# Kernel optimization log

Measured on AMD Instinct MI355X. Metric: run time of the kernel, lower is better.

Reference implementation:

```python
import jax, jax.numpy as jnp
import numpy as np

NUM_USERS = 50000
NUM_ITEMS = 100000
TOTAL_NODES = NUM_USERS + NUM_ITEMS
EMBED_DIM = 128
NUM_LAYERS = 2
NUM_EDGES = 2000000
REL_WEIGHTS = (1.0, 0.5, 2.0)  # rel_weight dict values, fixed order


def setup_inputs() -> dict:
    key = jax.random.key(0)
    ks = jax.random.split(key, 7)
    # Xavier-uniform embedding table
    bound = np.sqrt(6.0 / (TOTAL_NODES + EMBED_DIM))
    emb = jax.random.uniform(ks[0], (TOTAL_NODES, EMBED_DIM), jnp.float32, -bound, bound)
    inp = {"emb": emb}
    for r in range(3):
        inp[f"src_r{r}"] = jax.random.randint(ks[1 + 2 * r], (NUM_EDGES,), 0, TOTAL_NODES, jnp.int32)
        inp[f"dst_r{r}"] = jax.random.randint(ks[2 + 2 * r], (NUM_EDGES,), 0, TOTAL_NODES, jnp.int32)
    return inp


def _propagate(x, srcs, dsts):
    # One layer: agg = mean over relations of w_r * SpMM_r(x), where
    # SparseTensor(row=src, col=dst).matmul(x) => out[src] += x[dst]
    agg = jnp.zeros_like(x)
    for w, src, dst in zip(REL_WEIGHTS, srcs, dsts):
        msg = jax.ops.segment_sum(x[dst], src, num_segments=TOTAL_NODES)
        agg = agg + w * msg
    return agg / len(REL_WEIGHTS)


def reference(emb, src_r0, dst_r0, src_r1, dst_r1, src_r2, dst_r2):
    srcs = (src_r0, src_r1, src_r2)
    dsts = (dst_r0, dst_r1, dst_r2)
    x = emb
    all_embs = [x]
    for _ in range(NUM_LAYERS):
        x = _propagate(x, srcs, dsts)
        all_embs.append(x)
    z = jnp.mean(jnp.stack(all_embs, axis=1), axis=1)  # [N, D]
    users_emb = z[:NUM_USERS]
    items_emb = z[NUM_USERS:NUM_USERS + NUM_ITEMS]
    return users_emb, items_emb
```

## Files before the change

### kernel.cpp

```cpp
#include <hip/hip_runtime.h>
#include <hip/hip_fp16.h>

#define TOTAL_NODES 150000
#define EMBED_DIM   128
#define NUM_EDGES   2000000
#define N_ELEM      (TOTAL_NODES * EMBED_DIM)

#define NGRP     37
#define GCAP     180224
#define EPB1     4096
#define NBKT     2344
#define NBKT_PAD 2368
#define SCAP2    2944
#define P2BLK    44
#define BS_NODES 64

typedef float vf2 __attribute__((ext_vector_type(2)));
typedef float vf4 __attribute__((ext_vector_type(4)));

__global__ void convert_kernel(const float* __restrict__ in, __half* __restrict__ outh,
                               int* __restrict__ gcur, int* __restrict__ bcur) {
    const int n4 = N_ELEM / 4;
    const int stride = gridDim.x * blockDim.x;
    const int gid = blockIdx.x * blockDim.x + threadIdx.x;
    if (gid < NGRP) gcur[gid] = 0;
    if (gid < NBKT_PAD) bcur[gid] = 0;
    for (int i = gid; i < n4; i += stride) {
        float4 v = reinterpret_cast<const float4*>(in)[i];
        union { __half2 h[2]; vf2 f; } u;
        u.h[0] = __float22half2_rn({v.x, v.y});
        u.h[1] = __float22half2_rn({v.z, v.w});
        __builtin_nontemporal_store(u.f, reinterpret_cast<vf2*>(outh) + i);
    }
}

__global__ __launch_bounds__(256) void split1(const int* __restrict__ s0, const int* __restrict__ d0,
                                              const int* __restrict__ s1, const int* __restrict__ d1,
                                              const int* __restrict__ s2, const int* __restrict__ d2,
                                              int* __restrict__ gcur, unsigned int* __restrict__ gbuf) {
    const int rel   = blockIdx.x >> 9;
    const int inner = blockIdx.x & 511;
    const int base  = inner * EPB1;
    const int ne    = min(EPB1, NUM_EDGES - base);
    if (ne <= 0) return;
    const int* sp = (rel == 0) ? s0 : ((rel == 1) ? s1 : s2);
    const int* dp = (rel == 0) ? d0 : ((rel == 1) ? d1 : d2);

    __shared__ int cnt[NGRP], excl[NGRP], bas[NGRP], rc[NGRP];
    __shared__ unsigned int stage[EPB1];
    __shared__ unsigned char grp[EPB1];
    const int t = threadIdx.x;
    for (int i = t; i < NGRP; i += 256) cnt[i] = 0;
    __syncthreads();

    unsigned int pay[16];
    int pg[16];
    #pragma unroll
    for (int q = 0; q < 4; ++q) {
        const int idx = (q * 256 + t) * 4;
        if (idx < ne) {
            const int4 s4 = *reinterpret_cast<const int4*>(sp + base + idx);
            const int4 d4 = *reinterpret_cast<const int4*>(dp + base + idx);
            const int ss[4] = {s4.x, s4.y, s4.z, s4.w};
            const int dd[4] = {d4.x, d4.y, d4.z, d4.w};
            #pragma unroll
            for (int k = 0; k < 4; ++k) {
                const int g = ss[k] >> 12;
                pay[q * 4 + k] = ((unsigned int)(ss[k] & 4095) << 20) |
                                 ((unsigned int)dd[k] << 2) | (unsigned int)rel;
                pg[q * 4 + k] = g;
                atomicAdd(&cnt[g], 1);
            }
        }
    }
    __syncthreads();
    if (t == 0) { int run = 0; for (int i = 0; i < NGRP; ++i) { excl[i] = run; run += cnt[i]; } }
    __syncthreads();
    if (t < NGRP) { if (cnt[t] > 0) bas[t] = atomicAdd(&gcur[t], cnt[t]); rc[t] = excl[t]; }
    __syncthreads();
    #pragma unroll
    for (int q = 0; q < 4; ++q) {
        const int idx = (q * 256 + t) * 4;
        if (idx < ne) {
            #pragma unroll
            for (int k = 0; k < 4; ++k) {
                const int g = pg[q * 4 + k];
                const int pos = atomicAdd(&rc[g], 1);
                stage[pos] = pay[q * 4 + k];
                grp[pos] = (unsigned char)g;
            }
        }
    }
    __syncthreads();
    for (int j = t; j < ne; j += 256) {
        const int g = grp[j];
        const int o = bas[g] + (j - excl[g]);
        if (o < GCAP) gbuf[(size_t)g * GCAP + o] = stage[j];
    }
}

__global__ __launch_bounds__(256) void split2(const int* __restrict__ gcur,
                                              const unsigned int* __restrict__ gbuf,
                                              int* __restrict__ bcur, unsigned int* __restrict__ buf2) {
    const int g     = blockIdx.x / P2BLK;
    const int inner = blockIdx.x % P2BLK;
    const int gsz   = min(gcur[g], GCAP);
    const int base  = inner * EPB1;
    if (base >= gsz) return;
    const int ne = min(EPB1, gsz - base);
    const unsigned int* src = gbuf + (size_t)g * GCAP + base;

    __shared__ int cnt[64], excl[64], bas2[64], rc[64];
    __shared__ unsigned int stage[EPB1];
    const int t = threadIdx.x;
    if (t < 64) cnt[t] = 0;
    __syncthreads();

    unsigned int pay[16];
    #pragma unroll
    for (int q = 0; q < 4; ++q) {
        const int idx = (q * 256 + t) * 4;
        if (idx + 4 <= ne) {
            const uint4 v = *reinterpret_cast<const uint4*>(src + idx);
            pay[q * 4 + 0] = v.x; pay[q * 4 + 1] = v.y;
            pay[q * 4 + 2] = v.z; pay[q * 4 + 3] = v.w;
            atomicAdd(&cnt[(v.x >> 26) & 63], 1);
            atomicAdd(&cnt[(v.y >> 26) & 63], 1);
            atomicAdd(&cnt[(v.z >> 26) & 63], 1);
            atomicAdd(&cnt[(v.w >> 26) & 63], 1);
        } else {
            #pragma unroll
            for (int k = 0; k < 4; ++k) {
                if (idx + k < ne) {
                    const unsigned int p = src[idx + k];
                    pay[q * 4 + k] = p;
                    atomicAdd(&cnt[(p >> 26) & 63], 1);
                }
            }
        }
    }
    __syncthreads();
    if (t == 0) { int run = 0; for (int i = 0; i < 64; ++i) { excl[i] = run; run += cnt[i]; } }
    __syncthreads();
    if (t < 64) { if (cnt[t] > 0) bas2[t] = atomicAdd(&bcur[g * 64 + t], cnt[t]); rc[t] = excl[t]; }
    __syncthreads();
    #pragma unroll
    for (int q = 0; q < 4; ++q) {
        const int idx = (q * 256 + t) * 4;
        #pragma unroll
        for (int k = 0; k < 4; ++k) {
            if (idx + k < ne) {
                const unsigned int p = pay[q * 4 + k];
                const int pos = atomicAdd(&rc[(p >> 26) & 63], 1);
                stage[pos] = p;
            }
        }
    }
    __syncthreads();
    for (int j = t; j < ne; j += 256) {
        const unsigned int p = stage[j];
        const int bb = (p >> 26) & 63;
        const int o = bas2[bb] + (j - excl[bb]);
        if (o < SCAP2) buf2[(size_t)(g * 64 + bb) * SCAP2 + o] = p;
    }
}

template <int MODE>
__global__ __launch_bounds__(256) void pull_kernel(const __half* __restrict__ xh,
                                                   const int* __restrict__ bcur,
                                                   const unsigned int* __restrict__ buf2,
                                                   const float* __restrict__ embf,
                                                   __half* __restrict__ aggh,
                                                   float* __restrict__ outf) {
    __shared__ unsigned int sorted[SCAP2];
    __shared__ int cnt[64], cur[64], noff[65];
    const int b = blockIdx.x, t = threadIdx.x;
    const int c = min(bcur[b], SCAP2);
    const unsigned int* rb = buf2 + (size_t)b * SCAP2;
    if (t < 64) cnt[t] = 0;
    __syncthreads();
    for (int i = t; i < c; i += 256) atomicAdd(&cnt[(rb[i] >> 20) & 63], 1);
    __syncthreads();
    if (t == 0) { int run = 0; for (int i = 0; i < 64; ++i) { noff[i] = run; run += cnt[i]; } noff[64] = run; }
    __syncthreads();
    if (t < 64) cur[t] = noff[t];
    __syncthreads();
    for (int i = t; i < c; i += 256) {
        const unsigned int p = rb[i];
        const int pos = atomicAdd(&cur[(p >> 20) & 63], 1);
        sorted[pos] = p & 0xFFFFFu;
    }
    __syncthreads();

    const int hw = t >> 5, lane = t & 31;
    const int sub = lane >> 4, ch = lane & 15;
    const char* xb = reinterpret_cast<const char*>(xh) + (ch << 4);
    union F4H { vf4 f; __half2 h[4]; };
    const float c1 = 1.f / 3.f, c2 = 1.f / 9.f, c3 = 1.f / 27.f;

#define EDGE_FMA(P, W, ACC0, ACC1) do {                                         \
        F4H _u; _u.f = *reinterpret_cast<const vf4*>(xb + ((size_t)((P) >> 2) << 8)); \
        float2 _x0 = __half22float2(_u.h[0]), _x1 = __half22float2(_u.h[1]);    \
        float2 _x2 = __half22float2(_u.h[2]), _x3 = __half22float2(_u.h[3]);    \
        ACC0.x = fmaf(W, _x0.x, ACC0.x); ACC0.y = fmaf(W, _x0.y, ACC0.y);       \
        ACC0.z = fmaf(W, _x1.x, ACC0.z); ACC0.w = fmaf(W, _x1.y, ACC0.w);       \
        ACC1.x = fmaf(W, _x2.x, ACC1.x); ACC1.y = fmaf(W, _x2.y, ACC1.y);       \
        ACC1.z = fmaf(W, _x3.x, ACC1.z); ACC1.w = fmaf(W, _x3.y, ACC1.w);       \
    } while (0)
#define REL_W(P) ((((P) & 3u) == 1u) ? 0.5f : ((((P) & 3u) == 2u) ? 2.0f : 1.0f))

    for (int ln = hw; ln < BS_NODES; ln += 8) {
        const int node = b * BS_NODES + ln;
        if (node >= TOTAL_NODES) break;
        vf4 a0 = {0.f, 0.f, 0.f, 0.f}, b0 = {0.f, 0.f, 0.f, 0.f};
        vf4 a1 = {0.f, 0.f, 0.f, 0.f}, b1 = {0.f, 0.f, 0.f, 0.f};
        int i = noff[ln];
        const int e1 = noff[ln + 1];
        for (; i + 8 <= e1; i += 8) {
            const unsigned int p0 = sorted[i + sub];
            const unsigned int p1 = sorted[i + 2 + sub];
            const unsigned int p2 = sorted[i + 4 + sub];
            const unsigned int p3 = sorted[i + 6 + sub];
            const float w0 = REL_W(p0), w1 = REL_W(p1), w2 = REL_W(p2), w3 = REL_W(p3);
            EDGE_FMA(p0, w0, a0, a1);
            EDGE_FMA(p1, w1, b0, b1);
            EDGE_FMA(p2, w2, a0, a1);
            EDGE_FMA(p3, w3, b0, b1);
        }
        for (; i + 2 <= e1; i += 2) {
            const unsigned int p = sorted[i + sub];
            const float w = REL_W(p);
            EDGE_FMA(p, w, a0, a1);
        }
        if (i < e1) {
            const unsigned int p = sorted[i];
            const float w = sub ? 0.f : REL_W(p);
            EDGE_FMA(p, w, a0, a1);
        }
        a0 += b0; a1 += b1;
        a0.x += __shfl_xor(a0.x, 16); a0.y += __shfl_xor(a0.y, 16);
        a0.z += __shfl_xor(a0.z, 16); a0.w += __shfl_xor(a0.w, 16);
        a1.x += __shfl_xor(a1.x, 16); a1.y += __shfl_xor(a1.y, 16);
        a1.z += __shfl_xor(a1.z, 16); a1.w += __shfl_xor(a1.w, 16);
        if (sub == 0) {
            if (MODE == 0) {
                F4H o;
                o.h[0] = __float22half2_rn({a0.x, a0.y});
                o.h[1] = __float22half2_rn({a0.z, a0.w});
                o.h[2] = __float22half2_rn({a1.x, a1.y});
                o.h[3] = __float22half2_rn({a1.z, a1.w});
                __builtin_nontemporal_store(o.f,
                    reinterpret_cast<vf4*>(reinterpret_cast<char*>(aggh) + ((size_t)node << 8) + (ch << 4)));
            } else {
                const float* ep = embf + (size_t)node * EMBED_DIM + ch * 8;
                const float4 e0 = *reinterpret_cast<const float4*>(ep);
                const float4 e1v = *reinterpret_cast<const float4*>(ep + 4);
                F4H av;
                av.f = *reinterpret_cast<const vf4*>(
                    reinterpret_cast<const char*>(xh) + ((size_t)node << 8) + (ch << 4));
                const float2 g0 = __half22float2(av.h[0]), g1 = __half22float2(av.h[1]);
                const float2 g2 = __half22float2(av.h[2]), g3 = __half22float2(av.h[3]);
                vf4 z0, z1;
                z0.x = e0.x * c1 + g0.x * c2 + a0.x * c3;
                z0.y = e0.y * c1 + g0.y * c2 + a0.y * c3;
                z0.z = e0.z * c1 + g1.x * c2 + a0.z * c3;
                z0.w = e0.w * c1 + g1.y * c2 + a0.w * c3;
                z1.x = e1v.x * c1 + g2.x * c2 + a1.x * c3;
                z1.y = e1v.y * c1 + g2.y * c2 + a1.y * c3;
                z1.z = e1v.z * c1 + g3.x * c2 + a1.z * c3;
                z1.w = e1v.w * c1 + g3.y * c2 + a1.w * c3;
                float* op = outf + (size_t)node * EMBED_DIM + ch * 8;
                __builtin_nontemporal_store(z0, reinterpret_cast<vf4*>(op));
                __builtin_nontemporal_store(z1, reinterpret_cast<vf4*>(op + 4));
            }
        }
    }
#undef EDGE_FMA
#undef REL_W
}

extern "C" void kernel_launch(void* const* d_in, const int* in_sizes, int n_in,
                              void* d_out, int out_size, void* d_ws, size_t ws_size,
                              hipStream_t stream) {
    const float* emb = (const float*)d_in[0];
    const int* s0 = (const int*)d_in[1];
    const int* d0 = (const int*)d_in[2];
    const int* s1 = (const int*)d_in[3];
    const int* d1 = (const int*)d_in[4];
    const int* s2 = (const int*)d_in[5];
    const int* d2 = (const int*)d_in[6];
    float* out = (float*)d_out;
    __half* embh = (__half*)d_out;

    char* ws = (char*)d_ws;
    __half*       aggh = (__half*)ws;            ws += (size_t)N_ELEM * 2;
    int*          gcur = (int*)ws;               ws += 64 * 4;
    int*          bcur = (int*)ws;               ws += (size_t)NBKT_PAD * 4;
    unsigned int* gbuf = (unsigned int*)ws;      ws += (size_t)NGRP * GCAP * 4;
    unsigned int* buf2 = (unsigned int*)ws;

    convert_kernel<<<2048, 256, 0, stream>>>(emb, embh, gcur, bcur);
    split1<<<3 * 512, 256, 0, stream>>>(s0, d0, s1, d1, s2, d2, gcur, gbuf);
    split2<<<NGRP * P2BLK, 256, 0, stream>>>(gcur, gbuf, bcur, buf2);

    pull_kernel<0><<<NBKT, 256, 0, stream>>>(embh, bcur, buf2, nullptr, aggh, nullptr);
    pull_kernel<1><<<NBKT, 256, 0, stream>>>(aggh, bcur, buf2, emb, nullptr, out);
}
```

Baseline: 665.4 us.

## Remap pull gather to full-row 32-lane loads and enlarge split blocks

The pull kernel now has each 32-lane half-wave read a full 256-byte fp16 row per edge, one 8-byte chunk per lane. Previously the edges were split across two 16-lane subgroups with 16-byte loads, followed by a shuffle reduction. The inner loop is unrolled to 8 edges with two accumulators, and the cross-subgroup shuffles are gone. The split kernels also move to 512 threads and 8192 edges per block, halving the number of blocks and global atomics. The trade-off is smaller per-lane loads, which may reduce memory-level parallelism per request, and larger shared-memory staging per block.

```diff
diff --git a/kernel.cpp b/kernel.cpp
--- a/kernel.cpp
+++ b/kernel.cpp
@@ -8,11 +8,12 @@
 
 #define NGRP     37
 #define GCAP     180224
-#define EPB1     4096
+#define EPB      8192
+#define S1BLK    256
 #define NBKT     2344
 #define NBKT_PAD 2368
 #define SCAP2    2944
-#define P2BLK    44
+#define P2BLK    22
 #define BS_NODES 64
 
 typedef float vf2 __attribute__((ext_vector_type(2)));
@@ -34,30 +35,30 @@
     }
 }
 
-__global__ __launch_bounds__(256) void split1(const int* __restrict__ s0, const int* __restrict__ d0,
+__global__ __launch_bounds__(512) void split1(const int* __restrict__ s0, const int* __restrict__ d0,
                                               const int* __restrict__ s1, const int* __restrict__ d1,
                                               const int* __restrict__ s2, const int* __restrict__ d2,
                                               int* __restrict__ gcur, unsigned int* __restrict__ gbuf) {
-    const int rel   = blockIdx.x >> 9;
-    const int inner = blockIdx.x & 511;
-    const int base  = inner * EPB1;
-    const int ne    = min(EPB1, NUM_EDGES - base);
+    const int rel   = blockIdx.x >> 8;
+    const int inner = blockIdx.x & (S1BLK - 1);
+    const int base  = inner * EPB;
+    const int ne    = min(EPB, NUM_EDGES - base);
     if (ne <= 0) return;
     const int* sp = (rel == 0) ? s0 : ((rel == 1) ? s1 : s2);
     const int* dp = (rel == 0) ? d0 : ((rel == 1) ? d1 : d2);
 
     __shared__ int cnt[NGRP], excl[NGRP], bas[NGRP], rc[NGRP];
-    __shared__ unsigned int stage[EPB1];
-    __shared__ unsigned char grp[EPB1];
+    __shared__ unsigned int stage[EPB];
+    __shared__ unsigned char grp[EPB];
     const int t = threadIdx.x;
-    for (int i = t; i < NGRP; i += 256) cnt[i] = 0;
+    if (t < NGRP) cnt[t] = 0;
     __syncthreads();
 
     unsigned int pay[16];
     int pg[16];
     #pragma unroll
     for (int q = 0; q < 4; ++q) {
-        const int idx = (q * 256 + t) * 4;
+        const int idx = (q * 512 + t) * 4;
         if (idx < ne) {
             const int4 s4 = *reinterpret_cast<const int4*>(sp + base + idx);
             const int4 d4 = *reinterpret_cast<const int4*>(dp + base + idx);
@@ -80,7 +81,7 @@
     __syncthreads();
     #pragma unroll
     for (int q = 0; q < 4; ++q) {
-        const int idx = (q * 256 + t) * 4;
+        const int idx = (q * 512 + t) * 4;
         if (idx < ne) {
             #pragma unroll
             for (int k = 0; k < 4; ++k) {
@@ -92,26 +93,26 @@
         }
     }
     __syncthreads();
-    for (int j = t; j < ne; j += 256) {
+    for (int j = t; j < ne; j += 512) {
         const int g = grp[j];
         const int o = bas[g] + (j - excl[g]);
         if (o < GCAP) gbuf[(size_t)g * GCAP + o] = stage[j];
     }
 }
 
-__global__ __launch_bounds__(256) void split2(const int* __restrict__ gcur,
+__global__ __launch_bounds__(512) void split2(const int* __restrict__ gcur,
                                               const unsigned int* __restrict__ gbuf,
                                               int* __restrict__ bcur, unsigned int* __restrict__ buf2) {
     const int g     = blockIdx.x / P2BLK;
     const int inner = blockIdx.x % P2BLK;
     const int gsz   = min(gcur[g], GCAP);
-    const int base  = inner * EPB1;
+    const int base  = inner * EPB;
     if (base >= gsz) return;
-    const int ne = min(EPB1, gsz - base);
+    const int ne = min(EPB, gsz - base);
     const unsigned int* src = gbuf + (size_t)g * GCAP + base;
 
     __shared__ int cnt[64], excl[64], bas2[64], rc[64];
-    __shared__ unsigned int stage[EPB1];
+    __shared__ unsigned int stage[EPB];
     const int t = threadIdx.x;
     if (t < 64) cnt[t] = 0;
     __syncthreads();
@@ -119,7 +120,7 @@
     unsigned int pay[16];
     #pragma unroll
     for (int q = 0; q < 4; ++q) {
-        const int idx = (q * 256 + t) * 4;
+        const int idx = (q * 512 + t) * 4;
         if (idx + 4 <= ne) {
             const uint4 v = *reinterpret_cast<const uint4*>(src + idx);
             pay[q * 4 + 0] = v.x; pay[q * 4 + 1] = v.y;
@@ -146,7 +147,7 @@
     __syncthreads();
     #pragma unroll
     for (int q = 0; q < 4; ++q) {
-        const int idx = (q * 256 + t) * 4;
+        const int idx = (q * 512 + t) * 4;
         #pragma unroll
         for (int k = 0; k < 4; ++k) {
             if (idx + k < ne) {
@@ -157,7 +158,7 @@
         }
     }
     __syncthreads();
-    for (int j = t; j < ne; j += 256) {
+    for (int j = t; j < ne; j += 512) {
         const unsigned int p = stage[j];
         const int bb = (p >> 26) & 63;
         const int o = bas2[bb] + (j - excl[bb]);
@@ -193,89 +194,90 @@
     __syncthreads();
 
     const int hw = t >> 5, lane = t & 31;
-    const int sub = lane >> 4, ch = lane & 15;
-    const char* xb = reinterpret_cast<const char*>(xh) + (ch << 4);
-    union F4H { vf4 f; __half2 h[4]; };
-    const float c1 = 1.f / 3.f, c2 = 1.f / 9.f, c3 = 1.f / 27.f;
-
-#define EDGE_FMA(P, W, ACC0, ACC1) do {                                         \
-        F4H _u; _u.f = *reinterpret_cast<const vf4*>(xb + ((size_t)((P) >> 2) << 8)); \
-        float2 _x0 = __half22float2(_u.h[0]), _x1 = __half22float2(_u.h[1]);    \
-        float2 _x2 = __half22float2(_u.h[2]), _x3 = __half22float2(_u.h[3]);    \
-        ACC0.x = fmaf(W, _x0.x, ACC0.x); ACC0.y = fmaf(W, _x0.y, ACC0.y);       \
-        ACC0.z = fmaf(W, _x1.x, ACC0.z); ACC0.w = fmaf(W, _x1.y, ACC0.w);       \
-        ACC1.x = fmaf(W, _x2.x, ACC1.x); ACC1.y = fmaf(W, _x2.y, ACC1.y);       \
-        ACC1.z = fmaf(W, _x3.x, ACC1.z); ACC1.w = fmaf(W, _x3.y, ACC1.w);       \
-    } while (0)
+    const char* xb = reinterpret_cast<const char*>(xh) + (lane << 3);
+    union F2H { vf2 f; __half2 h[2]; };
 #define REL_W(P) ((((P) & 3u) == 1u) ? 0.5f : ((((P) & 3u) == 2u) ? 2.0f : 1.0f))
-
     for (int ln = hw; ln < BS_NODES; ln += 8) {
         const int node = b * BS_NODES + ln;
         if (node >= TOTAL_NODES) break;
-        vf4 a0 = {0.f, 0.f, 0.f, 0.f}, b0 = {0.f, 0.f, 0.f, 0.f};
-        vf4 a1 = {0.f, 0.f, 0.f, 0.f}, b1 = {0.f, 0.f, 0.f, 0.f};
+        vf4 acc0 = {0.f, 0.f, 0.f, 0.f};
+        vf4 acc1 = {0.f, 0.f, 0.f, 0.f};
         int i = noff[ln];
         const int e1 = noff[ln + 1];
         for (; i + 8 <= e1; i += 8) {
-            const unsigned int p0 = sorted[i + sub];
-            const unsigned int p1 = sorted[i + 2 + sub];
-            const unsigned int p2 = sorted[i + 4 + sub];
-            const unsigned int p3 = sorted[i + 6 + sub];
+            const unsigned int p0 = sorted[i + 0], p1 = sorted[i + 1];
+            const unsigned int p2 = sorted[i + 2], p3 = sorted[i + 3];
+            const unsigned int p4 = sorted[i + 4], p5 = sorted[i + 5];
+            const unsigned int p6 = sorted[i + 6], p7 = sorted[i + 7];
+            F2H u0, u1, u2, u3, u4, u5, u6, u7;
+            u0.f = *reinterpret_cast<const vf2*>(xb + ((size_t)(p0 >> 2) << 8));
+            u1.f = *reinterpret_cast<const vf2*>(xb + ((size_t)(p1 >> 2) << 8));
+            u2.f = *reinterpret_cast<const vf2*>(xb + ((size_t)(p2 >> 2) << 8));
+            u3.f = *reinterpret_cast<const vf2*>(xb + ((size_t)(p3 >> 2) << 8));
+            u4.f = *reinterpret_cast<const vf2*>(xb + ((size_t)(p4 >> 2) << 8));
+            u5.f = *reinterpret_cast<const vf2*>(xb + ((size_t)(p5 >> 2) << 8));
+            u6.f = *reinterpret_cast<const vf2*>(xb + ((size_t)(p6 >> 2) << 8));
+            u7.f = *reinterpret_cast<const vf2*>(xb + ((size_t)(p7 >> 2) << 8));
             const float w0 = REL_W(p0), w1 = REL_W(p1), w2 = REL_W(p2), w3 = REL_W(p3);
-            EDGE_FMA(p0, w0, a0, a1);
-            EDGE_FMA(p1, w1, b0, b1);
-            EDGE_FMA(p2, w2, a0, a1);
-            EDGE_FMA(p3, w3, b0, b1);
-        }
-        for (; i + 2 <= e1; i += 2) {
-            const unsigned int p = sorted[i + sub];
+            const float w4 = REL_W(p4), w5 = REL_W(p5), w6 = REL_W(p6), w7 = REL_W(p7);
+            float2 f0a = __half22float2(u0.h[0]), f0b = __half22float2(u0.h[1]);
+            float2 f1a = __half22float2(u1.h[0]), f1b = __half22float2(u1.h[1]);
+            float2 f2a = __half22float2(u2.h[0]), f2b = __half22float2(u2.h[1]);
+            float2 f3a = __half22float2(u3.h[0]), f3b = __half22float2(u3.h[1]);
+            float2 f4a = __half22float2(u4.h[0]), f4b = __half22float2(u4.h[1]);
+            float2 f5a = __half22float2(u5.h[0]), f5b = __half22float2(u5.h[1]);
+            float2 f6a = __half22float2(u6.h[0]), f6b = __half22float2(u6.h[1]);
+            float2 f7a = __half22float2(u7.h[0]), f7b = __half22float2(u7.h[1]);
+            acc0.x = fmaf(w0, f0a.x, acc0.x); acc0.y = fmaf(w0, f0a.y, acc0.y);
+            acc0.z = fmaf(w0, f0b.x, acc0.z); acc0.w = fmaf(w0, f0b.y, acc0.w);
+            acc1.x = fmaf(w1, f1a.x, acc1.x); acc1.y = fmaf(w1, f1a.y, acc1.y);
+            acc1.z = fmaf(w1, f1b.x, acc1.z); acc1.w = fmaf(w1, f1b.y, acc1.w);
+            acc0.x = fmaf(w2, f2a.x, acc0.x); acc0.y = fmaf(w2, f2a.y, acc0.y);
+            acc0.z = fmaf(w2, f2b.x, acc0.z); acc0.w = fmaf(w2, f2b.y, acc0.w);
+            acc1.x = fmaf(w3, f3a.x, acc1.x); acc1.y = fmaf(w3, f3a.y, acc1.y);
+            acc1.z = fmaf(w3, f3b.x, acc1.z); acc1.w = fmaf(w3, f3b.y, acc1.w);
+            acc0.x = fmaf(w4, f4a.x, acc0.x); acc0.y = fmaf(w4, f4a.y, acc0.y);
+            acc0.z = fmaf(w4, f4b.x, acc0.z); acc0.w = fmaf(w4, f4b.y, acc0.w);
+            acc1.x = fmaf(w5, f5a.x, acc1.x); acc1.y = fmaf(w5, f5a.y, acc1.y);
+            acc1.z = fmaf(w5, f5b.x, acc1.z); acc1.w = fmaf(w5, f5b.y, acc1.w);
+            acc0.x = fmaf(w6, f6a.x, acc0.x); acc0.y = fmaf(w6, f6a.y, acc0.y);
+            acc0.z = fmaf(w6, f6b.x, acc0.z); acc0.w = fmaf(w6, f6b.y, acc0.w);
+            acc1.x = fmaf(w7, f7a.x, acc1.x); acc1.y = fmaf(w7, f7a.y, acc1.y);
+            acc1.z = fmaf(w7, f7b.x, acc1.z); acc1.w = fmaf(w7, f7b.y, acc1.w);
+        }
+        for (; i < e1; ++i) {
+            const unsigned int p = sorted[i];
             const float w = REL_W(p);
-            EDGE_FMA(p, w, a0, a1);
-        }
-        if (i < e1) {
-            const unsigned int p = sorted[i];
-            const float w = sub ? 0.f : REL_W(p);
-            EDGE_FMA(p, w, a0, a1);
-        }
-        a0 += b0; a1 += b1;
-        a0.x += __shfl_xor(a0.x, 16); a0.y += __shfl_xor(a0.y, 16);
-        a0.z += __shfl_xor(a0.z, 16); a0.w += __shfl_xor(a0.w, 16);
-        a1.x += __shfl_xor(a1.x, 16); a1.y += __shfl_xor(a1.y, 16);
-        a1.z += __shfl_xor(a1.z, 16); a1.w += __shfl_xor(a1.w, 16);
-        if (sub == 0) {
-            if (MODE == 0) {
-                F4H o;
-                o.h[0] = __float22half2_rn({a0.x, a0.y});
-                o.h[1] = __float22half2_rn({a0.z, a0.w});
-                o.h[2] = __float22half2_rn({a1.x, a1.y});
-                o.h[3] = __float22half2_rn({a1.z, a1.w});
-                __builtin_nontemporal_store(o.f,
-                    reinterpret_cast<vf4*>(reinterpret_cast<char*>(aggh) + ((size_t)node << 8) + (ch << 4)));
-            } else {
-                const float* ep = embf + (size_t)node * EMBED_DIM + ch * 8;
-                const float4 e0 = *reinterpret_cast<const float4*>(ep);
-                const float4 e1v = *reinterpret_cast<const float4*>(ep + 4);
-                F4H av;
-                av.f = *reinterpret_cast<const vf4*>(
-                    reinterpret_cast<const char*>(xh) + ((size_t)node << 8) + (ch << 4));
-                const float2 g0 = __half22float2(av.h[0]), g1 = __half22float2(av.h[1]);
-                const float2 g2 = __half22float2(av.h[2]), g3 = __half22float2(av.h[3]);
-                vf4 z0, z1;
-                z0.x = e0.x * c1 + g0.x * c2 + a0.x * c3;
-                z0.y = e0.y * c1 + g0.y * c2 + a0.y * c3;
-                z0.z = e0.z * c1 + g1.x * c2 + a0.z * c3;
-                z0.w = e0.w * c1 + g1.y * c2 + a0.w * c3;
-                z1.x = e1v.x * c1 + g2.x * c2 + a1.x * c3;
-                z1.y = e1v.y * c1 + g2.y * c2 + a1.y * c3;
-                z1.z = e1v.z * c1 + g3.x * c2 + a1.z * c3;
-                z1.w = e1v.w * c1 + g3.y * c2 + a1.w * c3;
-                float* op = outf + (size_t)node * EMBED_DIM + ch * 8;
-                __builtin_nontemporal_store(z0, reinterpret_cast<vf4*>(op));
-                __builtin_nontemporal_store(z1, reinterpret_cast<vf4*>(op + 4));
-            }
-        }
-    }
-#undef EDGE_FMA
+            F2H u;
+            u.f = *reinterpret_cast<const vf2*>(xb + ((size_t)(p >> 2) << 8));
+            float2 fa = __half22float2(u.h[0]), fb = __half22float2(u.h[1]);
+            acc0.x = fmaf(w, fa.x, acc0.x); acc0.y = fmaf(w, fa.y, acc0.y);
+            acc0.z = fmaf(w, fb.x, acc0.z); acc0.w = fmaf(w, fb.y, acc0.w);
+        }
+        vf4 acc = acc0 + acc1;
+        if (MODE == 0) {
+            F2H o;
+            o.h[0] = __float22half2_rn({acc.x, acc.y});
+            o.h[1] = __float22half2_rn({acc.z, acc.w});
+            __builtin_nontemporal_store(o.f,
+                reinterpret_cast<vf2*>(reinterpret_cast<char*>(aggh) + (((size_t)node) << 8) + (lane << 3)));
+        } else {
+            const float4 e = *reinterpret_cast<const float4*>(embf + (size_t)node * EMBED_DIM + lane * 4);
+            F2H a;
+            a.f = *reinterpret_cast<const vf2*>(
+                reinterpret_cast<const char*>(xh) + (((size_t)node) << 8) + (lane << 3));
+            float2 a0 = __half22float2(a.h[0]);
+            float2 a1 = __half22float2(a.h[1]);
+            const float c1 = 1.f / 3.f, c2 = 1.f / 9.f, c3 = 1.f / 27.f;
+            vf4 z;
+            z.x = e.x * c1 + a0.x * c2 + acc.x * c3;
+            z.y = e.y * c1 + a0.y * c2 + acc.y * c3;
+            z.z = e.z * c1 + a1.x * c2 + acc.z * c3;
+            z.w = e.w * c1 + a1.y * c2 + acc.w * c3;
+            __builtin_nontemporal_store(z,
+                reinterpret_cast<vf4*>(outf + (size_t)node * EMBED_DIM + lane * 4));
+        }
+    }
 #undef REL_W
 }
 
@@ -300,8 +302,8 @@
     unsigned int* buf2 = (unsigned int*)ws;
 
     convert_kernel<<<2048, 256, 0, stream>>>(emb, embh, gcur, bcur);
-    split1<<<3 * 512, 256, 0, stream>>>(s0, d0, s1, d1, s2, d2, gcur, gbuf);
-    split2<<<NGRP * P2BLK, 256, 0, stream>>>(gcur, gbuf, bcur, buf2);
+    split1<<<3 * S1BLK, 512, 0, stream>>>(s0, d0, s1, d1, s2, d2, gcur, gbuf);
+    split2<<<NGRP * P2BLK, 512, 0, stream>>>(gcur, gbuf, bcur, buf2);
 
     pull_kernel<0><<<NBKT, 256, 0, stream>>>(embh, bcur, buf2, nullptr, aggh, nullptr);
     pull_kernel<1><<<NBKT, 256, 0, stream>>>(aggh, bcur, buf2, emb, nullptr, out);
```

New measurement: 645.7 us. -3.0%, faster.
